# Optimization experiments

Measured on AMD Instinct MI355X. Metric: run time of the kernel, lower is better.

The kernel has to match this reference:

```python
import jax, jax.numpy as jnp
import numpy as np

B, T, I, H, K, U = 16, 256, 64, 128, 64, 256
NOISE_INIT = 0.1

def lecun_tanh(x):
    return 1.7159 * jnp.tanh(0.666 * x)

def setup_inputs() -> dict:
    key = jax.random.key(0)
    ks = jax.random.split(key, 16)
    s_in = 1.0 / np.sqrt(I + H)
    s_bb = 1.0 / np.sqrt(U)
    inp = {
        "x": jax.random.normal(ks[0], (B, T, I), dtype=jnp.float32),
        "timespans": jax.random.uniform(ks[1], (B, T), dtype=jnp.float32, minval=0.05, maxval=1.0),
        "noise_eps": jax.random.normal(ks[2], (T, B, K, H), dtype=jnp.float32),
        # backbone: Linear(I+H -> U)
        "Wb": jax.random.normal(ks[3], (I + H, U), dtype=jnp.float32) * s_in,
        "bb": jnp.zeros((U,), dtype=jnp.float32),
        # CfC heads: Linear(U -> H) each
        "W_ff1": jax.random.normal(ks[4], (U, H), dtype=jnp.float32) * s_bb,
        "b_ff1": jnp.zeros((H,), dtype=jnp.float32),
        "W_ff2": jax.random.normal(ks[5], (U, H), dtype=jnp.float32) * s_bb,
        "b_ff2": jnp.zeros((H,), dtype=jnp.float32),
        "W_ta": jax.random.normal(ks[6], (U, H), dtype=jnp.float32) * s_bb,
        "b_ta": jnp.zeros((H,), dtype=jnp.float32),
        "W_tb": jax.random.normal(ks[7], (U, H), dtype=jnp.float32) * s_bb,
        "b_tb": jnp.zeros((H,), dtype=jnp.float32),
        # learnable time-scaled noise scale (per hidden unit)
        "noise_scale": jnp.full((H,), NOISE_INIT, dtype=jnp.float32),
    }
    return inp


def reference(x, timespans, noise_eps, Wb, bb, W_ff1, b_ff1, W_ff2, b_ff2,
              W_ta, b_ta, W_tb, b_tb, noise_scale):
    # initial particle state: zeros, uniform log-weights
    particles0 = jnp.zeros((B, K, H), dtype=x.dtype)
    log_w0 = jnp.full((B, K), -jnp.log(jnp.asarray(K, x.dtype)), dtype=x.dtype)

    def step(carry, inputs):
        particles, log_w = carry
        x_t, ts_t, eps_t = inputs  # [B,I], [B], [B,K,H]
        ts = ts_t[:, None, None]                                  # [B,1,1]
        xk = jnp.broadcast_to(x_t[:, None, :], (B, K, I))
        z = jnp.concatenate([xk, particles], axis=-1)             # [B,K,I+H]
        bbk = lecun_tanh(jnp.einsum('bku,uv->bkv', z, Wb) + bb)   # backbone [B,K,U]
        ff1 = jnp.tanh(jnp.einsum('bku,uh->bkh', bbk, W_ff1) + b_ff1)
        ff2 = jnp.tanh(jnp.einsum('bku,uh->bkh', bbk, W_ff2) + b_ff2)
        t_a = jnp.einsum('bku,uh->bkh', bbk, W_ta) + b_ta
        t_b = jnp.einsum('bku,uh->bkh', bbk, W_tb) + b_tb
        t_interp = jax.nn.sigmoid(t_a * ts + t_b)                 # CfC gate
        new_p = ff1 * (1.0 - t_interp) + t_interp * ff2           # [B,K,H]
        # time-scaled state noise injection
        new_p = new_p + noise_scale * jnp.sqrt(ts) * eps_t
        # weights stay uniform (no observations) -> ESS = K, no resampling
        w = jax.nn.softmax(log_w, axis=-1)                        # [B,K]
        out = jnp.einsum('bk,bkh->bh', w, new_p)                  # weighted mean
        return (new_p, log_w), out

    x_t = jnp.transpose(x, (1, 0, 2))        # [T,B,I]
    ts_t = jnp.transpose(timespans, (1, 0))  # [T,B]
    (particles, log_w), outs = jax.lax.scan(step, (particles0, log_w0),
                                            (x_t, ts_t, noise_eps))
    outputs = jnp.transpose(outs, (1, 0, 2))  # [B,T,H]
    return outputs, particles, log_w
```

## Files before the change

kernel.cpp:

```cpp
#include <hip/hip_runtime.h>
#include <math.h>

typedef __attribute__((ext_vector_type(8))) short short8;
typedef __attribute__((ext_vector_type(4))) float f32x4;

#define B_ 16
#define T_ 256
#define I_ 64
#define H_ 128
#define K_ 64
#define U_ 256
#define KC 16
#define NTHR 512

#define OUT_OFF_P (B_*T_*H_)
#define OUT_OFF_LW (OUT_OFF_P + B_*K_*H_)

__device__ __forceinline__ unsigned short f2bf(float x) {
    unsigned int u = __float_as_uint(x);
    u += 0x7fffu + ((u >> 16) & 1u);
    return (unsigned short)(u >> 16);
}
__device__ __forceinline__ float fast_tanh(float x) {
    float e = __expf(2.0f * x);
    return 1.0f - 2.0f * __builtin_amdgcn_rcpf(e + 1.0f);
}
__device__ __forceinline__ float fast_sigmoid(float x) {
    return __builtin_amdgcn_rcpf(1.0f + __expf(-x));
}
__device__ __forceinline__ unsigned int swz_p(unsigned int row, unsigned int col) {
    unsigned int byte = row * 256u + col * 2u;
    byte ^= (row & 7u) << 4;
    return byte >> 1;
}
__device__ __forceinline__ unsigned int swz_b(unsigned int row, unsigned int col) {
    unsigned int byte = row * 512u + col * 2u;
    byte ^= (row & 7u) << 4;
    return byte >> 1;
}

#define BAR() do { asm volatile("s_waitcnt lgkmcnt(0)" ::: "memory"); \
                   __builtin_amdgcn_s_barrier(); \
                   __builtin_amdgcn_sched_barrier(0); } while (0)

#define MFMA16(a, bfrag, c) __builtin_amdgcn_mfma_f32_16x16x32_bf16((a), (bfrag), (c), 0, 0, 0)

__global__ __launch_bounds__(NTHR, 2) void pf_kernel(
    const float* __restrict__ x, const float* __restrict__ tspan,
    const float* __restrict__ eps, const float* __restrict__ Wb,
    const float* __restrict__ bb,
    const float* __restrict__ Wf1, const float* __restrict__ bf1,
    const float* __restrict__ Wf2, const float* __restrict__ bf2,
    const float* __restrict__ Wta, const float* __restrict__ bta,
    const float* __restrict__ Wtb, const float* __restrict__ btb,
    const float* __restrict__ nscale, float* __restrict__ out)
{
    const int tid  = threadIdx.x;
    const int lane = tid & 63;
    const int wv   = tid >> 6;
    const int ln15 = lane & 15;
    const int l4   = lane >> 4;
    const int bid  = blockIdx.x;
    const int b    = bid >> 2;
    const int k0   = (bid & 3) * KC;

    __shared__ unsigned short p_bf[KC * H_];
    __shared__ unsigned short bbk_bf[KC * U_];
    __shared__ unsigned short x_bf[T_ * I_];
    __shared__ float ts_lds[T_];

    for (int i = tid; i < KC * H_; i += NTHR) p_bf[i] = 0;
    for (int i = tid; i < T_ * I_; i += NTHR) x_bf[i] = f2bf(x[b * (T_ * I_) + i]);
    for (int i = tid; i < T_; i += NTHR) ts_lds[i] = tspan[b * T_ + i];

    short8 B1[6][2];
    #pragma unroll
    for (int kt = 0; kt < 6; ++kt) {
        #pragma unroll
        for (int ct = 0; ct < 2; ++ct) {
            short8 f;
            const int col = wv * 32 + ct * 16 + ln15;
            #pragma unroll
            for (int j = 0; j < 8; ++j) f[j] = (short)f2bf(Wb[(kt * 32 + l4 * 8 + j) * U_ + col]);
            B1[kt][ct] = f;
        }
    }
    float bias1[2];
    #pragma unroll
    for (int ct = 0; ct < 2; ++ct) bias1[ct] = bb[wv * 32 + ct * 16 + ln15];

    const float* Whp[4] = {Wf1, Wf2, Wta, Wtb};
    const int hc = wv * 16 + ln15;
    short8 B2[4][8];
    #pragma unroll
    for (int hd = 0; hd < 4; ++hd) {
        #pragma unroll
        for (int kt = 0; kt < 8; ++kt) {
            short8 f;
            #pragma unroll
            for (int j = 0; j < 8; ++j) f[j] = (short)f2bf(Whp[hd][(kt * 32 + l4 * 8 + j) * H_ + hc]);
            B2[hd][kt] = f;
        }
    }
    const float bf1c = bf1[hc], bf2c = bf2[hc];
    const float btac = bta[hc], btbc = btb[hc];
    const float nscc = nscale[hc];

    #pragma unroll
    for (int kt = 0; kt < 6; ++kt) asm volatile("" : "+v"(B1[kt][0]), "+v"(B1[kt][1]));
    #pragma unroll
    for (int hd = 0; hd < 4; ++hd) {
        #pragma unroll
        for (int kt = 0; kt < 8; ++kt) asm volatile("" : "+v"(B2[hd][kt]));
    }

    if ((bid & 3) == 0 && tid < K_)
        out[OUT_OFF_LW + b * K_ + tid] = -4.1588830833596715f;

    __syncthreads();

    const float* ep0 = eps + ((size_t)(b * K_ + k0 + l4 * 4)) * H_ + hc;
    float ecur[4];
    #pragma unroll
    for (int r = 0; r < 4; ++r) ecur[r] = ep0[r * H_];
    float tscur = ts_lds[0];

    const f32x4 zero4 = {0.f, 0.f, 0.f, 0.f};

    for (int t = 0; t < T_; ++t) {
        const int tn = (t + 1 < T_) ? t + 1 : t;
        const float* epn = ep0 + (size_t)tn * (B_ * K_ * H_);
        float enext[4];
        #pragma unroll
        for (int r = 0; r < 4; ++r) enext[r] = epn[r * H_];
        const float tsn = ts_lds[tn];

        f32x4 acc0 = zero4, acc1 = zero4;
        const short8 ax0 = *(const short8*)&x_bf[t * I_ + l4 * 8];
        const short8 ax1 = *(const short8*)&x_bf[t * I_ + 32 + l4 * 8];
        acc0 = MFMA16(ax0, B1[0][0], acc0); acc1 = MFMA16(ax0, B1[0][1], acc1);
        acc0 = MFMA16(ax1, B1[1][0], acc0); acc1 = MFMA16(ax1, B1[1][1], acc1);
        #pragma unroll
        for (int kt = 0; kt < 4; ++kt) {
            const short8 ap = *(const short8*)&p_bf[swz_p(ln15, kt * 32 + l4 * 8)];
            acc0 = MFMA16(ap, B1[2 + kt][0], acc0);
            acc1 = MFMA16(ap, B1[2 + kt][1], acc1);
        }
        #pragma unroll
        for (int r = 0; r < 4; ++r) {
            const int row = l4 * 4 + r;
            bbk_bf[swz_b(row, wv * 32 + ln15)]      = f2bf(1.7159f * fast_tanh(0.666f * (acc0[r] + bias1[0])));
            bbk_bf[swz_b(row, wv * 32 + 16 + ln15)] = f2bf(1.7159f * fast_tanh(0.666f * (acc1[r] + bias1[1])));
        }
        BAR();

        f32x4 a_f1 = zero4, a_f2 = zero4, a_ta = zero4, a_tb = zero4;
        #pragma unroll
        for (int kt = 0; kt < 8; ++kt) {
            const short8 a = *(const short8*)&bbk_bf[swz_b(ln15, kt * 32 + l4 * 8)];
            a_f1 = MFMA16(a, B2[0][kt], a_f1);
            a_f2 = MFMA16(a, B2[1][kt], a_f2);
            a_ta = MFMA16(a, B2[2][kt], a_ta);
            a_tb = MFMA16(a, B2[3][kt], a_tb);
        }
        const float sq = sqrtf(tscur);
        float psum = 0.f;
        #pragma unroll
        for (int r = 0; r < 4; ++r) {
            const int row = l4 * 4 + r;
            const float f1v = fast_tanh(a_f1[r] + bf1c);
            const float f2v = fast_tanh(a_f2[r] + bf2c);
            const float tiv = fast_sigmoid((a_ta[r] + btac) * tscur + (a_tb[r] + btbc));
            const float np  = f1v + tiv * (f2v - f1v) + nscc * sq * ecur[r];
            p_bf[swz_p(row, hc)] = f2bf(np);
            psum += np;
            if (t == T_ - 1)
                out[OUT_OFF_P + (size_t)(b * K_ + k0 + row) * H_ + hc] = np;
        }
        psum += __shfl_xor(psum, 16);
        psum += __shfl_xor(psum, 32);
        if (lane < 16)
            atomicAdd(&out[(size_t)(b * T_ + t) * H_ + wv * 16 + lane], psum * (1.0f / 64.0f));

        #pragma unroll
        for (int r = 0; r < 4; ++r) ecur[r] = enext[r];
        tscur = tsn;
        BAR();
    }
}

extern "C" void kernel_launch(void* const* d_in, const int* in_sizes, int n_in,
                              void* d_out, int out_size, void* d_ws, size_t ws_size,
                              hipStream_t stream) {
    const float* x    = (const float*)d_in[0];
    const float* tsp  = (const float*)d_in[1];
    const float* eps  = (const float*)d_in[2];
    const float* Wb   = (const float*)d_in[3];
    const float* bb   = (const float*)d_in[4];
    const float* Wf1  = (const float*)d_in[5];
    const float* bf1  = (const float*)d_in[6];
    const float* Wf2  = (const float*)d_in[7];
    const float* bf2  = (const float*)d_in[8];
    const float* Wta  = (const float*)d_in[9];
    const float* bta  = (const float*)d_in[10];
    const float* Wtb  = (const float*)d_in[11];
    const float* btb  = (const float*)d_in[12];
    const float* nsc  = (const float*)d_in[13];
    float* out = (float*)d_out;

    (void)hipMemsetAsync(d_out, 0, (size_t)OUT_OFF_P * sizeof(float), stream);
    pf_kernel<<<dim3(64), dim3(NTHR), 0, stream>>>(
        x, tsp, eps, Wb, bb, Wf1, bf1, Wf2, bf2, Wta, bta, Wtb, btb, nsc, out);
}
```

Baseline: 552.8 us.

## Precompute next-step x projection, defer atomics, pack bbk stores, improve LDS swizzle

Moves the input-projection MFMAs for step t+1 to the end of step t, off the critical path that follows the barrier. The per-step output atomicAdd is deferred to the start of the next iteration so it overlaps other work. Backbone activations are written as packed 32-bit pairs, with a matching permutation of the K index in the head weights and an extra swizzle bit to cut LDS bank conflicts. s_setprio is raised around the head MFMA block. The permuted weight layout must stay consistent with the new store pattern, and the added xacc/psum state raises register pressure.

```diff
diff --git a/kernel.cpp b/kernel.cpp
--- a/kernel.cpp
+++ b/kernel.cpp
@@ -28,15 +28,13 @@
 __device__ __forceinline__ float fast_sigmoid(float x) {
     return __builtin_amdgcn_rcpf(1.0f + __expf(-x));
 }
-__device__ __forceinline__ unsigned int swz_p(unsigned int row, unsigned int col) {
+__device__ __forceinline__ unsigned int swzbyte_p(unsigned int row, unsigned int col) {
     unsigned int byte = row * 256u + col * 2u;
-    byte ^= (row & 7u) << 4;
-    return byte >> 1;
-}
-__device__ __forceinline__ unsigned int swz_b(unsigned int row, unsigned int col) {
-    unsigned int byte = row * 512u + col * 2u;
-    byte ^= (row & 7u) << 4;
-    return byte >> 1;
+    return byte ^ ((row & 7u) << 4) ^ ((row & 8u) << 2);
+}
+__device__ __forceinline__ unsigned int swzbyte_b(unsigned int row, unsigned int pos) {
+    unsigned int byte = row * 512u + pos * 2u;
+    return byte ^ ((row & 7u) << 4) ^ ((row & 8u) << 2);
 }
 
 #define BAR() do { asm volatile("s_waitcnt lgkmcnt(0)" ::: "memory"); \
@@ -98,7 +96,11 @@
         for (int kt = 0; kt < 8; ++kt) {
             short8 f;
             #pragma unroll
-            for (int j = 0; j < 8; ++j) f[j] = (short)f2bf(Whp[hd][(kt * 32 + l4 * 8 + j) * H_ + hc]);
+            for (int j = 0; j < 8; ++j) {
+                const int pos = l4 * 8 + j;
+                const int kg  = kt * 32 + (pos >> 1) + ((pos & 1) << 4);
+                f[j] = (short)f2bf(Whp[hd][kg * H_ + hc]);
+            }
             B2[hd][kt] = f;
         }
     }
@@ -127,7 +129,25 @@
 
     const f32x4 zero4 = {0.f, 0.f, 0.f, 0.f};
 
+    f32x4 xacc0, xacc1;
+    {
+        const short8 ax0 = *(const short8*)&x_bf[0 * I_ + l4 * 8];
+        const short8 ax1 = *(const short8*)&x_bf[0 * I_ + 32 + l4 * 8];
+        xacc0 = MFMA16(ax0, B1[0][0], zero4); xacc1 = MFMA16(ax0, B1[0][1], zero4);
+        xacc0 = MFMA16(ax1, B1[1][0], xacc0); xacc1 = MFMA16(ax1, B1[1][1], xacc1);
+    }
+    float psum_d = 0.f;
+
+    #pragma unroll 1
     for (int t = 0; t < T_; ++t) {
+        if (t) {
+            float ps = psum_d;
+            ps += __shfl_xor(ps, 16);
+            ps += __shfl_xor(ps, 32);
+            if (lane < 16)
+                atomicAdd(&out[(size_t)(b * T_ + (t - 1)) * H_ + wv * 16 + lane], ps * (1.0f / 64.0f));
+        }
+
         const int tn = (t + 1 < T_) ? t + 1 : t;
         const float* epn = ep0 + (size_t)tn * (B_ * K_ * H_);
         float enext[4];
@@ -135,36 +155,37 @@
         for (int r = 0; r < 4; ++r) enext[r] = epn[r * H_];
         const float tsn = ts_lds[tn];
 
-        f32x4 acc0 = zero4, acc1 = zero4;
-        const short8 ax0 = *(const short8*)&x_bf[t * I_ + l4 * 8];
-        const short8 ax1 = *(const short8*)&x_bf[t * I_ + 32 + l4 * 8];
-        acc0 = MFMA16(ax0, B1[0][0], acc0); acc1 = MFMA16(ax0, B1[0][1], acc1);
-        acc0 = MFMA16(ax1, B1[1][0], acc0); acc1 = MFMA16(ax1, B1[1][1], acc1);
+        f32x4 acc0 = xacc0, acc1 = xacc1;
         #pragma unroll
         for (int kt = 0; kt < 4; ++kt) {
-            const short8 ap = *(const short8*)&p_bf[swz_p(ln15, kt * 32 + l4 * 8)];
+            const short8 ap = *(const short8*)((const char*)p_bf + swzbyte_p(ln15, kt * 32 + l4 * 8));
             acc0 = MFMA16(ap, B1[2 + kt][0], acc0);
             acc1 = MFMA16(ap, B1[2 + kt][1], acc1);
         }
         #pragma unroll
         for (int r = 0; r < 4; ++r) {
             const int row = l4 * 4 + r;
-            bbk_bf[swz_b(row, wv * 32 + ln15)]      = f2bf(1.7159f * fast_tanh(0.666f * (acc0[r] + bias1[0])));
-            bbk_bf[swz_b(row, wv * 32 + 16 + ln15)] = f2bf(1.7159f * fast_tanh(0.666f * (acc1[r] + bias1[1])));
+            const unsigned int p0 = f2bf(1.7159f * fast_tanh(0.666f * (acc0[r] + bias1[0])));
+            const unsigned int p1 = f2bf(1.7159f * fast_tanh(0.666f * (acc1[r] + bias1[1])));
+            *(unsigned int*)((char*)bbk_bf + swzbyte_b(row, wv * 32 + 2 * ln15)) = p0 | (p1 << 16);
         }
         BAR();
 
+        __builtin_amdgcn_s_setprio(1);
         f32x4 a_f1 = zero4, a_f2 = zero4, a_ta = zero4, a_tb = zero4;
         #pragma unroll
         for (int kt = 0; kt < 8; ++kt) {
-            const short8 a = *(const short8*)&bbk_bf[swz_b(ln15, kt * 32 + l4 * 8)];
+            const short8 a = *(const short8*)((const char*)bbk_bf + swzbyte_b(ln15, kt * 32 + l4 * 8));
             a_f1 = MFMA16(a, B2[0][kt], a_f1);
             a_f2 = MFMA16(a, B2[1][kt], a_f2);
             a_ta = MFMA16(a, B2[2][kt], a_ta);
             a_tb = MFMA16(a, B2[3][kt], a_tb);
         }
+        __builtin_amdgcn_s_setprio(0);
+
         const float sq = sqrtf(tscur);
         float psum = 0.f;
+        const bool last = (t == T_ - 1);
         #pragma unroll
         for (int r = 0; r < 4; ++r) {
             const int row = l4 * 4 + r;
@@ -172,20 +193,32 @@
             const float f2v = fast_tanh(a_f2[r] + bf2c);
             const float tiv = fast_sigmoid((a_ta[r] + btac) * tscur + (a_tb[r] + btbc));
             const float np  = f1v + tiv * (f2v - f1v) + nscc * sq * ecur[r];
-            p_bf[swz_p(row, hc)] = f2bf(np);
+            *(unsigned short*)((char*)p_bf + swzbyte_p(row, hc)) = f2bf(np);
             psum += np;
-            if (t == T_ - 1)
+            if (last)
                 out[OUT_OFF_P + (size_t)(b * K_ + k0 + row) * H_ + hc] = np;
         }
-        psum += __shfl_xor(psum, 16);
-        psum += __shfl_xor(psum, 32);
-        if (lane < 16)
-            atomicAdd(&out[(size_t)(b * T_ + t) * H_ + wv * 16 + lane], psum * (1.0f / 64.0f));
+        psum_d = psum;
+
+        {
+            const short8 axn0 = *(const short8*)&x_bf[tn * I_ + l4 * 8];
+            const short8 axn1 = *(const short8*)&x_bf[tn * I_ + 32 + l4 * 8];
+            xacc0 = MFMA16(axn0, B1[0][0], zero4); xacc1 = MFMA16(axn0, B1[0][1], zero4);
+            xacc0 = MFMA16(axn1, B1[1][0], xacc0); xacc1 = MFMA16(axn1, B1[1][1], xacc1);
+        }
 
         #pragma unroll
         for (int r = 0; r < 4; ++r) ecur[r] = enext[r];
         tscur = tsn;
         BAR();
+    }
+
+    {
+        float ps = psum_d;
+        ps += __shfl_xor(ps, 16);
+        ps += __shfl_xor(ps, 32);
+        if (lane < 16)
+            atomicAdd(&out[(size_t)(b * T_ + (T_ - 1)) * H_ + wv * 16 + lane], ps * (1.0f / 64.0f));
     }
 }
 
```

New measurement: 620.8 us. +12.3%, slower.

## Precompute x·Wb projection per batch and process two particle groups per block

Applied to the files above, without the earlier changes.

The input projection x_t·Wb[:I] plus bias is hoisted out of the recurrent loop and computed once per batch into LDS as bf16, so the per-step backbone only multiplies the particle state by Wb[I:]. Each block now handles 32 particles as two 16-row groups sharing the same register-resident weights, which halves the grid to 32 blocks and doubles the independent MFMA chains per step. This trades fewer blocks (less parallelism across CUs) for more ILP per wave and fewer barrier-bound steps in total. Rounding x·Wb+bias to bf16 adds a small extra precision loss.

```diff
diff --git a/kernel.cpp b/kernel.cpp
--- a/kernel.cpp
+++ b/kernel.cpp
@@ -11,6 +11,7 @@
 #define K_ 64
 #define U_ 256
 #define KC 16
+#define NG 2
 #define NTHR 512
 
 #define OUT_OFF_P (B_*T_*H_)
@@ -20,6 +21,9 @@
     unsigned int u = __float_as_uint(x);
     u += 0x7fffu + ((u >> 16) & 1u);
     return (unsigned short)(u >> 16);
+}
+__device__ __forceinline__ float bf2f(unsigned short u) {
+    return __uint_as_float(((unsigned int)u) << 16);
 }
 __device__ __forceinline__ float fast_tanh(float x) {
     float e = __expf(2.0f * x);
@@ -61,34 +65,30 @@
     const int ln15 = lane & 15;
     const int l4   = lane >> 4;
     const int bid  = blockIdx.x;
-    const int b    = bid >> 2;
-    const int k0   = (bid & 3) * KC;
-
-    __shared__ unsigned short p_bf[KC * H_];
-    __shared__ unsigned short bbk_bf[KC * U_];
-    __shared__ unsigned short x_bf[T_ * I_];
+    const int b    = bid >> 1;
+    const int k0   = (bid & 1) * (NG * KC);
+
+    __shared__ unsigned short xw_lds[T_ * U_];
+    __shared__ unsigned short p_bf[NG][KC * H_];
+    __shared__ unsigned short bbk_bf[NG][KC * U_];
     __shared__ float ts_lds[T_];
 
-    for (int i = tid; i < KC * H_; i += NTHR) p_bf[i] = 0;
-    for (int i = tid; i < T_ * I_; i += NTHR) x_bf[i] = f2bf(x[b * (T_ * I_) + i]);
+    for (int i = tid; i < NG * KC * H_; i += NTHR) ((unsigned short*)p_bf)[i] = 0;
     for (int i = tid; i < T_; i += NTHR) ts_lds[i] = tspan[b * T_ + i];
 
-    short8 B1[6][2];
-    #pragma unroll
-    for (int kt = 0; kt < 6; ++kt) {
+    short8 B1p[4][2];
+    #pragma unroll
+    for (int kt = 0; kt < 4; ++kt) {
         #pragma unroll
         for (int ct = 0; ct < 2; ++ct) {
             short8 f;
             const int col = wv * 32 + ct * 16 + ln15;
             #pragma unroll
-            for (int j = 0; j < 8; ++j) f[j] = (short)f2bf(Wb[(kt * 32 + l4 * 8 + j) * U_ + col]);
-            B1[kt][ct] = f;
-        }
-    }
-    float bias1[2];
-    #pragma unroll
-    for (int ct = 0; ct < 2; ++ct) bias1[ct] = bb[wv * 32 + ct * 16 + ln15];
-
+            for (int j = 0; j < 8; ++j)
+                f[j] = (short)f2bf(Wb[(I_ + kt * 32 + l4 * 8 + j) * U_ + col]);
+            B1p[kt][ct] = f;
+        }
+    }
     const float* Whp[4] = {Wf1, Wf2, Wta, Wtb};
     const int hc = wv * 16 + ln15;
     short8 B2[4][8];
@@ -98,7 +98,8 @@
         for (int kt = 0; kt < 8; ++kt) {
             short8 f;
             #pragma unroll
-            for (int j = 0; j < 8; ++j) f[j] = (short)f2bf(Whp[hd][(kt * 32 + l4 * 8 + j) * H_ + hc]);
+            for (int j = 0; j < 8; ++j)
+                f[j] = (short)f2bf(Whp[hd][(kt * 32 + l4 * 8 + j) * H_ + hc]);
             B2[hd][kt] = f;
         }
     }
@@ -106,76 +107,138 @@
     const float btac = bta[hc], btbc = btb[hc];
     const float nscc = nscale[hc];
 
-    #pragma unroll
-    for (int kt = 0; kt < 6; ++kt) asm volatile("" : "+v"(B1[kt][0]), "+v"(B1[kt][1]));
+    {
+        short8 Bx[2][2];
+        #pragma unroll
+        for (int kt = 0; kt < 2; ++kt) {
+            #pragma unroll
+            for (int ct = 0; ct < 2; ++ct) {
+                short8 f;
+                const int col = wv * 32 + ct * 16 + ln15;
+                #pragma unroll
+                for (int j = 0; j < 8; ++j)
+                    f[j] = (short)f2bf(Wb[(kt * 32 + l4 * 8 + j) * U_ + col]);
+                Bx[kt][ct] = f;
+            }
+        }
+        const float bbc0 = bb[wv * 32 + ln15];
+        const float bbc1 = bb[wv * 32 + 16 + ln15];
+        const f32x4 z4 = {0.f, 0.f, 0.f, 0.f};
+        for (int tt = 0; tt < 16; ++tt) {
+            const int t0 = tt * 16;
+            short8 axf[2];
+            #pragma unroll
+            for (int kt = 0; kt < 2; ++kt) {
+                const float* xp = &x[(size_t)(b * T_ + t0 + ln15) * I_ + kt * 32 + l4 * 8];
+                short8 f;
+                #pragma unroll
+                for (int j = 0; j < 8; ++j) f[j] = (short)f2bf(xp[j]);
+                axf[kt] = f;
+            }
+            f32x4 xa0 = z4, xa1 = z4;
+            xa0 = MFMA16(axf[0], Bx[0][0], xa0); xa1 = MFMA16(axf[0], Bx[0][1], xa1);
+            xa0 = MFMA16(axf[1], Bx[1][0], xa0); xa1 = MFMA16(axf[1], Bx[1][1], xa1);
+            #pragma unroll
+            for (int r = 0; r < 4; ++r) {
+                const int trow = t0 + l4 * 4 + r;
+                xw_lds[trow * U_ + wv * 32 + ln15]      = f2bf(xa0[r] + bbc0);
+                xw_lds[trow * U_ + wv * 32 + 16 + ln15] = f2bf(xa1[r] + bbc1);
+            }
+        }
+    }
+
+    #pragma unroll
+    for (int kt = 0; kt < 4; ++kt) asm volatile("" : "+v"(B1p[kt][0]), "+v"(B1p[kt][1]));
     #pragma unroll
     for (int hd = 0; hd < 4; ++hd) {
         #pragma unroll
         for (int kt = 0; kt < 8; ++kt) asm volatile("" : "+v"(B2[hd][kt]));
     }
 
-    if ((bid & 3) == 0 && tid < K_)
+    if ((bid & 1) == 0 && tid < K_)
         out[OUT_OFF_LW + b * K_ + tid] = -4.1588830833596715f;
 
     __syncthreads();
 
-    const float* ep0 = eps + ((size_t)(b * K_ + k0 + l4 * 4)) * H_ + hc;
-    float ecur[4];
-    #pragma unroll
-    for (int r = 0; r < 4; ++r) ecur[r] = ep0[r * H_];
+    const float* epg0 = eps + ((size_t)(b * K_ + k0 + 0 * KC + l4 * 4)) * H_ + hc;
+    const float* epg1 = eps + ((size_t)(b * K_ + k0 + 1 * KC + l4 * 4)) * H_ + hc;
+    float ec0[4], ec1[4];
+    #pragma unroll
+    for (int r = 0; r < 4; ++r) { ec0[r] = epg0[r * H_]; ec1[r] = epg1[r * H_]; }
     float tscur = ts_lds[0];
 
     const f32x4 zero4 = {0.f, 0.f, 0.f, 0.f};
 
     for (int t = 0; t < T_; ++t) {
         const int tn = (t + 1 < T_) ? t + 1 : t;
-        const float* epn = ep0 + (size_t)tn * (B_ * K_ * H_);
-        float enext[4];
-        #pragma unroll
-        for (int r = 0; r < 4; ++r) enext[r] = epn[r * H_];
+        const size_t soff = (size_t)tn * (B_ * K_ * H_);
+        float en0[4], en1[4];
+        #pragma unroll
+        for (int r = 0; r < 4; ++r) { en0[r] = epg0[soff + r * H_]; en1[r] = epg1[soff + r * H_]; }
         const float tsn = ts_lds[tn];
 
-        f32x4 acc0 = zero4, acc1 = zero4;
-        const short8 ax0 = *(const short8*)&x_bf[t * I_ + l4 * 8];
-        const short8 ax1 = *(const short8*)&x_bf[t * I_ + 32 + l4 * 8];
-        acc0 = MFMA16(ax0, B1[0][0], acc0); acc1 = MFMA16(ax0, B1[0][1], acc1);
-        acc0 = MFMA16(ax1, B1[1][0], acc0); acc1 = MFMA16(ax1, B1[1][1], acc1);
+        const float xw0 = bf2f(xw_lds[t * U_ + wv * 32 + ln15]);
+        const float xw1 = bf2f(xw_lds[t * U_ + wv * 32 + 16 + ln15]);
+        f32x4 a00 = {xw0, xw0, xw0, xw0}, a01 = {xw1, xw1, xw1, xw1};
+        f32x4 a10 = a00, a11 = a01;
         #pragma unroll
         for (int kt = 0; kt < 4; ++kt) {
-            const short8 ap = *(const short8*)&p_bf[swz_p(ln15, kt * 32 + l4 * 8)];
-            acc0 = MFMA16(ap, B1[2 + kt][0], acc0);
-            acc1 = MFMA16(ap, B1[2 + kt][1], acc1);
+            const short8 ap0 = *(const short8*)&p_bf[0][swz_p(ln15, kt * 32 + l4 * 8)];
+            const short8 ap1 = *(const short8*)&p_bf[1][swz_p(ln15, kt * 32 + l4 * 8)];
+            a00 = MFMA16(ap0, B1p[kt][0], a00);
+            a01 = MFMA16(ap0, B1p[kt][1], a01);
+            a10 = MFMA16(ap1, B1p[kt][0], a10);
+            a11 = MFMA16(ap1, B1p[kt][1], a11);
         }
         #pragma unroll
         for (int r = 0; r < 4; ++r) {
             const int row = l4 * 4 + r;
-            bbk_bf[swz_b(row, wv * 32 + ln15)]      = f2bf(1.7159f * fast_tanh(0.666f * (acc0[r] + bias1[0])));
-            bbk_bf[swz_b(row, wv * 32 + 16 + ln15)] = f2bf(1.7159f * fast_tanh(0.666f * (acc1[r] + bias1[1])));
+            bbk_bf[0][swz_b(row, wv * 32 + ln15)]      = f2bf(1.7159f * fast_tanh(0.666f * a00[r]));
+            bbk_bf[0][swz_b(row, wv * 32 + 16 + ln15)] = f2bf(1.7159f * fast_tanh(0.666f * a01[r]));
+            bbk_bf[1][swz_b(row, wv * 32 + ln15)]      = f2bf(1.7159f * fast_tanh(0.666f * a10[r]));
+            bbk_bf[1][swz_b(row, wv * 32 + 16 + ln15)] = f2bf(1.7159f * fast_tanh(0.666f * a11[r]));
         }
         BAR();
 
-        f32x4 a_f1 = zero4, a_f2 = zero4, a_ta = zero4, a_tb = zero4;
+        f32x4 f1a = zero4, f2a = zero4, taa = zero4, tba = zero4;
+        f32x4 f1b = zero4, f2b = zero4, tab = zero4, tbb = zero4;
         #pragma unroll
         for (int kt = 0; kt < 8; ++kt) {
-            const short8 a = *(const short8*)&bbk_bf[swz_b(ln15, kt * 32 + l4 * 8)];
-            a_f1 = MFMA16(a, B2[0][kt], a_f1);
-            a_f2 = MFMA16(a, B2[1][kt], a_f2);
-            a_ta = MFMA16(a, B2[2][kt], a_ta);
-            a_tb = MFMA16(a, B2[3][kt], a_tb);
+            const short8 qa = *(const short8*)&bbk_bf[0][swz_b(ln15, kt * 32 + l4 * 8)];
+            const short8 qb = *(const short8*)&bbk_bf[1][swz_b(ln15, kt * 32 + l4 * 8)];
+            f1a = MFMA16(qa, B2[0][kt], f1a);
+            f2a = MFMA16(qa, B2[1][kt], f2a);
+            taa = MFMA16(qa, B2[2][kt], taa);
+            tba = MFMA16(qa, B2[3][kt], tba);
+            f1b = MFMA16(qb, B2[0][kt], f1b);
+            f2b = MFMA16(qb, B2[1][kt], f2b);
+            tab = MFMA16(qb, B2[2][kt], tab);
+            tbb = MFMA16(qb, B2[3][kt], tbb);
         }
         const float sq = sqrtf(tscur);
         float psum = 0.f;
+        const bool last = (t == T_ - 1);
         #pragma unroll
         for (int r = 0; r < 4; ++r) {
             const int row = l4 * 4 + r;
-            const float f1v = fast_tanh(a_f1[r] + bf1c);
-            const float f2v = fast_tanh(a_f2[r] + bf2c);
-            const float tiv = fast_sigmoid((a_ta[r] + btac) * tscur + (a_tb[r] + btbc));
-            const float np  = f1v + tiv * (f2v - f1v) + nscc * sq * ecur[r];
-            p_bf[swz_p(row, hc)] = f2bf(np);
-            psum += np;
-            if (t == T_ - 1)
-                out[OUT_OFF_P + (size_t)(b * K_ + k0 + row) * H_ + hc] = np;
+            {
+                const float f1v = fast_tanh(f1a[r] + bf1c);
+                const float f2v = fast_tanh(f2a[r] + bf2c);
+                const float tiv = fast_sigmoid((taa[r] + btac) * tscur + (tba[r] + btbc));
+                const float np  = f1v + tiv * (f2v - f1v) + nscc * sq * ec0[r];
+                p_bf[0][swz_p(row, hc)] = f2bf(np);
+                psum += np;
+                if (last) out[OUT_OFF_P + (size_t)(b * K_ + k0 + row) * H_ + hc] = np;
+            }
+            {
+                const float f1v = fast_tanh(f1b[r] + bf1c);
+                const float f2v = fast_tanh(f2b[r] + bf2c);
+                const float tiv = fast_sigmoid((tab[r] + btac) * tscur + (tbb[r] + btbc));
+                const float np  = f1v + tiv * (f2v - f1v) + nscc * sq * ec1[r];
+                p_bf[1][swz_p(row, hc)] = f2bf(np);
+                psum += np;
+                if (last) out[OUT_OFF_P + (size_t)(b * K_ + k0 + KC + row) * H_ + hc] = np;
+            }
         }
         psum += __shfl_xor(psum, 16);
         psum += __shfl_xor(psum, 32);
@@ -183,7 +246,7 @@
             atomicAdd(&out[(size_t)(b * T_ + t) * H_ + wv * 16 + lane], psum * (1.0f / 64.0f));
 
         #pragma unroll
-        for (int r = 0; r < 4; ++r) ecur[r] = enext[r];
+        for (int r = 0; r < 4; ++r) { ec0[r] = en0[r]; ec1[r] = en1[r]; }
         tscur = tsn;
         BAR();
     }
@@ -209,6 +272,6 @@
     float* out = (float*)d_out;
 
     (void)hipMemsetAsync(d_out, 0, (size_t)OUT_OFF_P * sizeof(float), stream);
-    pf_kernel<<<dim3(64), dim3(NTHR), 0, stream>>>(
+    pf_kernel<<<dim3(32), dim3(NTHR), 0, stream>>>(
         x, tsp, eps, Wb, bb, Wf1, bf1, Wf2, bf2, Wta, bta, Wtb, btb, nsc, out);
 }
```

Result: slower. 1.007 ms (+82.2%).
